# Optimization experiments

Hardware: AMD Instinct MI355X
Metric: run time of the kernel (lower is better)

The kernel has to match this reference:

```python
import jax, jax.numpy as jnp
import numpy as np

N = 50000      # areaNum
E = 64         # embeddingsize
NE = 800000    # nonzeros of normalized adjacency
WK = 9         # walk_length + 1
L = 2          # args.L
TMP = 0.5      # args.choosing_tmp
BIAS = 1e-4


def _logistic_noise(k, shape):
    # eps ~ U(bias, 1-bias); noise = log(eps) - log(1-eps)
    u = jax.random.uniform(k, shape, minval=BIAS, maxval=1.0 - BIAS)
    return jnp.log(u) - jnp.log1p(-u)


def setup_inputs() -> dict:
    key = jax.random.key(0)
    ks = jax.random.split(key, 16)
    rng = np.random.default_rng(0)

    # ---- normalized sparse adjacency (D^-1/2 A D^-1/2), COO sorted by row ----
    row = np.sort(rng.integers(0, N, NE))
    col = rng.integers(0, N, NE)
    deg = np.bincount(row, minlength=N).astype(np.float32)
    dinv = np.where(deg > 0, deg ** -0.5, 0.0).astype(np.float32)
    vals = dinv[row] * dinv[col]

    # ---- random-walk mean-pooling adjacency, row-normalized ----
    rw_row = np.repeat(np.arange(N), WK)
    rw_col = rng.integers(0, N, N * WK)
    rw_col[::WK] = np.arange(N)  # walk starts at self
    rw_vals = np.full(N * WK, 1.0 / WK, dtype=np.float32)

    def lin(k, fan_in, shape):
        return jax.random.normal(k, shape, dtype=jnp.float32) / np.sqrt(fan_in)

    inp = {
        'x': jax.random.normal(ks[0], (N, E), dtype=jnp.float32),
        'vals': jnp.asarray(vals),
        'rw_vals': jnp.asarray(rw_vals),
        't_W1': lin(ks[1], 2 * E, (L, 2 * E, E)),
        't_b1': jnp.zeros((L, E), jnp.float32),
        't_W2': lin(ks[2], E, (L, E, 1)),
        't_b2': jnp.zeros((L, 1), jnp.float32),
        's_W1': lin(ks[3], E, (L, E, E)),
        's_b1': jnp.zeros((L, E), jnp.float32),
        's_W2': lin(ks[4], E, (L, E, 1)),
        's_b2': jnp.zeros((L, 1), jnp.float32),
        't_noise': _logistic_noise(ks[5], (L, NE)),
        's_noise': _logistic_noise(ks[6], (L, N, 1)),
        'row': jnp.asarray(row, dtype=jnp.int64) if jax.config.jax_enable_x64 else jnp.asarray(row, dtype=jnp.int32),
        'col': jnp.asarray(col, dtype=jnp.int32),
        'rw_row': jnp.asarray(rw_row, dtype=jnp.int32),
        'rw_col': jnp.asarray(rw_col, dtype=jnp.int32),
    }
    inp['row'] = jnp.asarray(row, dtype=jnp.int32)
    return inp


def reference(x, vals, rw_vals, t_W1, t_b1, t_W2, t_b2, s_W1, s_b1, s_W2, s_b2,
              t_noise, s_noise, row, col, rw_row, rw_col):
    n = x.shape[0]

    def spmm(r, c, v, h):  # sparse [n,n] @ dense [n,E]
        return jax.ops.segment_sum(v[:, None] * h[c], r, num_segments=n)

    # per-edge concat of ORIGINAL embeddings (same tensor every layer, as in source)
    t_cat = jnp.concatenate([x[row], x[col]], axis=-1)  # [nE, 2E]

    # --- mask-learning pass ---
    cur = x
    t_masks, s_masks = [], []
    for i in range(L):
        cur = spmm(row, col, vals, cur)
        t_h = jax.nn.relu(t_cat @ t_W1[i] + t_b1[i])
        t_logit = t_h @ t_W2[i] + t_b2[i]                      # [nE,1]
        t_m = jax.nn.sigmoid((t_noise[i][:, None] + t_logit) / TMP)[:, 0]
        t_masks.append(t_m)
        s_h = jax.nn.relu(cur @ s_W1[i] + s_b1[i])
        s_logit = s_h @ s_W2[i] + s_b2[i]                      # [N,1]
        s_masks.append(jax.nn.sigmoid((s_noise[i] + s_logit) / TMP))

    # --- t branch: gated spmm propagation, mean over layers ---
    cur_t = x
    acc_t = x
    for i in range(L):
        cur_t = spmm(row, col, vals * t_masks[i], cur_t)
        acc_t = acc_t + cur_t
    emb_t = acc_t / (L + 1)

    # --- s branch: gated mix with random-walk mean pooling, then spmm ---
    cur_s = x
    acc_s = x
    s_reg = jnp.float32(0.0)
    for i in range(L):
        mp = spmm(rw_row, rw_col, rw_vals, cur_s)
        cur_s = s_masks[i] * cur_s + (1.0 - s_masks[i]) * mp
        cur_s = spmm(row, col, vals, cur_s)
        acc_s = acc_s + cur_s
        s_reg = s_reg + s_masks[i].sum() / n
    emb_s = acc_s / (L + 1)
    s_reg = s_reg / L
    t_reg = jnp.float32(0.0)  # source never accumulates into t_reg
    return emb_t, emb_s, t_reg, s_reg, t_masks[-1]
```

## Files before the change

kernel.cpp:

```cpp
#include <hip/hip_runtime.h>

#define NNODES 50000
#define EDIM 64
#define WKLEN 9
#define NEDGE 800000
#define NPAD (NNODES + 64)

using bf16x8 = __attribute__((ext_vector_type(8))) __bf16;
using f32x4  = __attribute__((ext_vector_type(4))) float;

__device__ __align__(256) unsigned short g_xbf[NPAD * EDIM];
__device__ __align__(256) unsigned short g_ABh[NNODES * 128];
__device__ __align__(256) unsigned short g_c1h[NPAD * EDIM];
__device__ __align__(256) unsigned short g_c2h[NPAD * EDIM];
__device__ __align__(256) unsigned short g_g0h[NNODES * EDIM];
__device__ __align__(256) unsigned short g_sc1h[NNODES * EDIM];
__device__ __align__(256) unsigned short g_Pr[NNODES * 128];
__device__ __align__(256) unsigned short g_Pc[NNODES * 128];
__device__ __align__(256) float g_mt0[NEDGE];
__device__ __align__(256) float g_mt1[NEDGE];
__device__ __align__(256) float g_sm0[NNODES];
__device__ __align__(256) float g_sm1[NNODES];
__device__ __align__(256) int   g_rowptr[NNODES + 1];
__device__ __align__(256) unsigned short g_Tswz[2048 * 8];
__device__ __align__(256) unsigned short g_Sswz[1024 * 8];

__device__ __forceinline__ unsigned short f2bf(float f) {
    union { float f; unsigned int i; } v;
    v.f = f;
    unsigned int r = v.i + 0x7FFFu + ((v.i >> 16) & 1u);
    return (unsigned short)(r >> 16);
}
__device__ __forceinline__ float bf2f_lo(unsigned int u) {
    union { unsigned int i; float f; } v; v.i = u << 16; return v.f;
}
__device__ __forceinline__ float bf2f_hi(unsigned int u) {
    union { unsigned int i; float f; } v; v.i = u & 0xFFFF0000u; return v.f;
}

__global__ __launch_bounds__(256) void misc_kernel(
    const float* __restrict__ x, const float* __restrict__ tW1,
    const float* __restrict__ sW1, const int* __restrict__ row,
    int n, int nE)
{
    int bid = blockIdx.x, tid = threadIdx.x;
    if (bid < 1563) {
        int i = bid * 256 + tid;
        if (i < NNODES * EDIM / 8) {
            const float* src = x + i * 8;
            union { unsigned short s[8]; uint4 q; } u;
#pragma unroll
            for (int j = 0; j < 8; ++j) u.s[j] = f2bf(src[j]);
            *(uint4*)&g_xbf[i * 8] = u.q;
        }
    } else if (bid < 1759) {
        int i = (bid - 1563) * 256 + tid;
        if (i > n) return;
        int lo = 0, hi = nE;
        while (lo < hi) {
            int mid = (lo + hi) >> 1;
            if (row[mid] < i) lo = mid + 1; else hi = mid;
        }
        g_rowptr[i] = lo;
    } else if (bid < 1767) {
        int t = (bid - 1759) * 256 + tid;
        int s = t >> 9, f = (t >> 6) & 7, ln = t & 63;
        int li = s >> 1, half = s & 1, ks = f >> 2, nn = f & 3;
        int q = ln >> 4, mcl = ln & 15;
        union { unsigned short sv[8]; uint4 q4; } u;
#pragma unroll
        for (int j = 0; j < 8; ++j) {
            int kg = half * 64 + ks * 32 + q * 8 + j;
            u.sv[j] = f2bf(tW1[li * 8192 + kg * 64 + nn * 16 + mcl]);
        }
        *(uint4*)&g_Tswz[t * 8] = u.q4;
    } else {
        int t = (bid - 1767) * 256 + tid;
        int li = t >> 9, ks = (t >> 8) & 1, nn = (t >> 6) & 3, ln = t & 63;
        int q = ln >> 4, mcl = ln & 15;
        union { unsigned short sv[8]; uint4 q4; } u;
#pragma unroll
        for (int j = 0; j < 8; ++j)
            u.sv[j] = f2bf(sW1[li * 4096 + (ks * 32 + q * 8 + j) * 64 + nn * 16 + mcl]);
        *(uint4*)&g_Sswz[t * 8] = u.q4;
    }
}

__global__ __launch_bounds__(256) void prep2_kernel(int n)
{
    int tid = threadIdx.x;
    int wave = tid >> 6, lane = tid & 63;
    int mc = lane & 15, quad = lane >> 4;
    int nb = blockIdx.x * 64 + wave * 16;
    const unsigned short* bp = g_xbf + (nb + mc) * 64 + quad * 8;
    bf16x8 af0 = *(const bf16x8*)bp;
    bf16x8 af1 = *(const bf16x8*)(bp + 32);
    const f32x4 zero = {0.f, 0.f, 0.f, 0.f};
#pragma unroll
    for (int s = 0; s < 4; ++s) {
        int li = s >> 1, half = s & 1;
        f32x4 acc[4];
#pragma unroll
        for (int nn = 0; nn < 4; ++nn) acc[nn] = zero;
#pragma unroll
        for (int nn = 0; nn < 4; ++nn) {
            bf16x8 b0 = *(const bf16x8*)&g_Tswz[((s * 8 + nn) * 64 + lane) * 8];
            bf16x8 b1 = *(const bf16x8*)&g_Tswz[((s * 8 + 4 + nn) * 64 + lane) * 8];
            acc[nn] = __builtin_amdgcn_mfma_f32_16x16x32_bf16(af0, b0, acc[nn], 0, 0, 0);
            acc[nn] = __builtin_amdgcn_mfma_f32_16x16x32_bf16(af1, b1, acc[nn], 0, 0, 0);
        }
        unsigned short* dst = half ? g_Pc : g_Pr;
#pragma unroll
        for (int nn = 0; nn < 4; ++nn)
#pragma unroll
            for (int r = 0; r < 4; ++r) {
                int node = nb + quad * 4 + r;
                if (node < n)
                    dst[node * 128 + li * 64 + nn * 16 + mc] = f2bf(acc[nn][r]);
            }
    }
}

__global__ __launch_bounds__(256) void edge_mask_kernel(
    const float* __restrict__ tb1, const float* __restrict__ tW2,
    const float* __restrict__ tb2, const float* __restrict__ tnoise,
    const int* __restrict__ row, const int* __restrict__ col,
    float* __restrict__ mask_out, int nE)
{
    int tid = threadIdx.x;
    int lane = tid & 63;
    int sub = lane & 7;
    int eg = lane >> 3;
    int wv = (blockIdx.x * 256 + tid) >> 6;
    int e = wv * 8 + eg;

    float b1_0[8], b1_1[8], w2_0[8], w2_1[8];
    *(float4*)&b1_0[0] = *(const float4*)&tb1[sub * 8];
    *(float4*)&b1_0[4] = *(const float4*)&tb1[sub * 8 + 4];
    *(float4*)&b1_1[0] = *(const float4*)&tb1[64 + sub * 8];
    *(float4*)&b1_1[4] = *(const float4*)&tb1[64 + sub * 8 + 4];
    *(float4*)&w2_0[0] = *(const float4*)&tW2[sub * 8];
    *(float4*)&w2_0[4] = *(const float4*)&tW2[sub * 8 + 4];
    *(float4*)&w2_1[0] = *(const float4*)&tW2[64 + sub * 8];
    *(float4*)&w2_1[4] = *(const float4*)&tW2[64 + sub * 8 + 4];

    int rn = row[e], cn = col[e];
    uint4 qr0 = *(const uint4*)&g_Pr[rn * 128 + sub * 8];
    uint4 qr1 = *(const uint4*)&g_Pr[rn * 128 + 64 + sub * 8];
    uint4 qc0 = *(const uint4*)&g_Pc[cn * 128 + sub * 8];
    uint4 qc1 = *(const uint4*)&g_Pc[cn * 128 + 64 + sub * 8];

    float p0 = 0.f, p1 = 0.f;
    unsigned r0[4] = {qr0.x, qr0.y, qr0.z, qr0.w};
    unsigned r1[4] = {qr1.x, qr1.y, qr1.z, qr1.w};
    unsigned c0[4] = {qc0.x, qc0.y, qc0.z, qc0.w};
    unsigned c1[4] = {qc1.x, qc1.y, qc1.z, qc1.w};
#pragma unroll
    for (int k = 0; k < 4; ++k) {
        float hA = fmaxf(bf2f_lo(r0[k]) + bf2f_lo(c0[k]) + b1_0[2 * k], 0.f);
        float hB = fmaxf(bf2f_hi(r0[k]) + bf2f_hi(c0[k]) + b1_0[2 * k + 1], 0.f);
        p0 = fmaf(hA, w2_0[2 * k], p0);
        p0 = fmaf(hB, w2_0[2 * k + 1], p0);
        float gA = fmaxf(bf2f_lo(r1[k]) + bf2f_lo(c1[k]) + b1_1[2 * k], 0.f);
        float gB = fmaxf(bf2f_hi(r1[k]) + bf2f_hi(c1[k]) + b1_1[2 * k + 1], 0.f);
        p1 = fmaf(gA, w2_1[2 * k], p1);
        p1 = fmaf(gB, w2_1[2 * k + 1], p1);
    }
#pragma unroll
    for (int off = 1; off <= 4; off <<= 1) {
        p0 += __shfl_xor(p0, off, 64);
        p1 += __shfl_xor(p1, off, 64);
    }
    if (sub == 0) {
        float z0 = (tnoise[e] + p0 + tb2[0]) * 2.0f;
        float m0 = 1.0f / (1.0f + expf(-z0));
        g_mt0[e] = m0;
        float z1 = (tnoise[nE + e] + p1 + tb2[1]) * 2.0f;
        float m1 = 1.0f / (1.0f + expf(-z1));
        g_mt1[e] = m1;
        mask_out[e] = m1;
    }
}

__device__ __forceinline__ void nm_body(
    int bid, const unsigned short* __restrict__ cur, int li,
    const float* __restrict__ b1, const float* __restrict__ W2,
    const float* __restrict__ b2, const float* __restrict__ noise,
    float* __restrict__ smout, int n)
{
    int tid = threadIdx.x;
    int wave = tid >> 6, lane = tid & 63;
    int mc = lane & 15, quad = lane >> 4;
    int nb = bid * 64 + wave * 16;
    const unsigned short* basep = cur + (nb + mc) * 64 + quad * 8;
    bf16x8 af0 = *(const bf16x8*)basep;
    bf16x8 af1 = *(const bf16x8*)(basep + 32);
    f32x4 acc[4];
    const f32x4 zero = {0.f, 0.f, 0.f, 0.f};
#pragma unroll
    for (int nn = 0; nn < 4; ++nn) acc[nn] = zero;
#pragma unroll
    for (int nn = 0; nn < 4; ++nn) {
        bf16x8 b0 = *(const bf16x8*)&g_Sswz[((li * 8 + nn) * 64 + lane) * 8];
        bf16x8 b1f = *(const bf16x8*)&g_Sswz[((li * 8 + 4 + nn) * 64 + lane) * 8];
        acc[nn] = __builtin_amdgcn_mfma_f32_16x16x32_bf16(af0, b0, acc[nn], 0, 0, 0);
        acc[nn] = __builtin_amdgcn_mfma_f32_16x16x32_bf16(af1, b1f, acc[nn], 0, 0, 0);
    }
    float p[4];
#pragma unroll
    for (int r = 0; r < 4; ++r) {
        float s = 0.f;
#pragma unroll
        for (int nn = 0; nn < 4; ++nn) {
            float h = acc[nn][r] + b1[nn * 16 + mc];
            s = fmaf(fmaxf(h, 0.f), W2[nn * 16 + mc], s);
        }
        p[r] = s;
    }
#pragma unroll
    for (int off = 8; off >= 1; off >>= 1)
#pragma unroll
        for (int r = 0; r < 4; ++r) p[r] += __shfl_xor(p[r], off, 64);
    if (mc == 0) {
        float b2v = b2[0];
#pragma unroll
        for (int r = 0; r < 4; ++r) {
            int node = nb + quad * 4 + r;
            if (node < n) {
                float z = (noise[node] + p[r] + b2v) * 2.0f;
                smout[node] = 1.0f / (1.0f + expf(-z));
            }
        }
    }
}

__global__ __launch_bounds__(256) void s1_kernel(
    const int* __restrict__ colv, const float* __restrict__ vals, int n)
{
    int w = (blockIdx.x * 256 + threadIdx.x) >> 6;
    int lane = threadIdx.x & 63;
    int el = lane >> 5, d2 = lane & 31;
    int s = g_rowptr[w], e = g_rowptr[w + 1];
    float p0 = 0.f, p1 = 0.f, q0 = 0.f, q1 = 0.f;
    float P0 = 0.f, P1 = 0.f, Q0 = 0.f, Q1 = 0.f;
    int j = s + el;
    for (; j + 2 < e; j += 4) {
        int cA = colv[j];      float vA = vals[j];     float mA = g_mt0[j];
        int cB = colv[j + 2];  float vB = vals[j + 2]; float mB = g_mt0[j + 2];
        unsigned uA = *(const unsigned*)&g_xbf[cA * 64 + 2 * d2];
        unsigned uB = *(const unsigned*)&g_xbf[cB * 64 + 2 * d2];
        float a0 = bf2f_lo(uA), a1 = bf2f_hi(uA);
        float bb0 = bf2f_lo(uB), bb1 = bf2f_hi(uB);
        float vmA = vA * mA, vmB = vB * mB;
        p0 = fmaf(vA, a0, p0);  p1 = fmaf(vA, a1, p1);
        q0 = fmaf(vmA, a0, q0); q1 = fmaf(vmA, a1, q1);
        P0 = fmaf(vB, bb0, P0);  P1 = fmaf(vB, bb1, P1);
        Q0 = fmaf(vmB, bb0, Q0); Q1 = fmaf(vmB, bb1, Q1);
    }
    for (; j < e; j += 2) {
        int c = colv[j]; float v = vals[j], m = g_mt0[j];
        unsigned u = *(const unsigned*)&g_xbf[c * 64 + 2 * d2];
        float a0 = bf2f_lo(u), a1 = bf2f_hi(u);
        float vm = v * m;
        p0 = fmaf(v, a0, p0);  p1 = fmaf(v, a1, p1);
        q0 = fmaf(vm, a0, q0); q1 = fmaf(vm, a1, q1);
    }
    p0 += P0; p1 += P1; q0 += Q0; q1 += Q1;
    p0 += __shfl_xor(p0, 32, 64); p1 += __shfl_xor(p1, 32, 64);
    q0 += __shfl_xor(q0, 32, 64); q1 += __shfl_xor(q1, 32, 64);
    if (el == 0) {
        uint2 pk;
        pk.x = (unsigned)f2bf(p0) | ((unsigned)f2bf(q0) << 16);
        pk.y = (unsigned)f2bf(p1) | ((unsigned)f2bf(q1) << 16);
        *(uint2*)&g_ABh[w * 128 + 4 * d2] = pk;
        *(unsigned*)&g_c1h[w * 64 + 2 * d2] =
            (unsigned)f2bf(p0) | ((unsigned)f2bf(p1) << 16);
    }
}

__global__ __launch_bounds__(256) void s2_nm0_kernel(
    const int* __restrict__ colv, const float* __restrict__ vals,
    const float* __restrict__ x, float* __restrict__ emb_t,
    const float* __restrict__ sb1, const float* __restrict__ sW2,
    const float* __restrict__ sb2, const float* __restrict__ snz, int n)
{
    if (blockIdx.x >= 12500) {
        nm_body(blockIdx.x - 12500, g_c1h, 0, sb1, sW2, sb2, snz, g_sm0, n);
        return;
    }
    int w = (blockIdx.x * 256 + threadIdx.x) >> 6;
    int lane = threadIdx.x & 63;
    int el = lane >> 5, d2 = lane & 31;
    int s = g_rowptr[w], e = g_rowptr[w + 1];
    float c0 = 0.f, c1 = 0.f, t0 = 0.f, t1 = 0.f;
    float C0 = 0.f, C1 = 0.f, T0 = 0.f, T1 = 0.f;
    int j = s + el;
    for (; j + 2 < e; j += 4) {
        int cA = colv[j];      float vA = vals[j];     float mA = g_mt1[j];
        int cB = colv[j + 2];  float vB = vals[j + 2]; float mB = g_mt1[j + 2];
        uint2 UA = *(const uint2*)&g_ABh[cA * 128 + 4 * d2];
        uint2 UB = *(const uint2*)&g_ABh[cB * 128 + 4 * d2];
        float vmA = vA * mA, vmB = vB * mB;
        c0 = fmaf(vA, bf2f_lo(UA.x), c0); t0 = fmaf(vmA, bf2f_hi(UA.x), t0);
        c1 = fmaf(vA, bf2f_lo(UA.y), c1); t1 = fmaf(vmA, bf2f_hi(UA.y), t1);
        C0 = fmaf(vB, bf2f_lo(UB.x), C0); T0 = fmaf(vmB, bf2f_hi(UB.x), T0);
        C1 = fmaf(vB, bf2f_lo(UB.y), C1); T1 = fmaf(vmB, bf2f_hi(UB.y), T1);
    }
    for (; j < e; j += 2) {
        int c = colv[j]; float v = vals[j], m = g_mt1[j];
        uint2 U = *(const uint2*)&g_ABh[c * 128 + 4 * d2];
        float vm = v * m;
        c0 = fmaf(v, bf2f_lo(U.x), c0); t0 = fmaf(vm, bf2f_hi(U.x), t0);
        c1 = fmaf(v, bf2f_lo(U.y), c1); t1 = fmaf(vm, bf2f_hi(U.y), t1);
    }
    c0 += C0; c1 += C1; t0 += T0; t1 += T1;
    c0 += __shfl_xor(c0, 32, 64); c1 += __shfl_xor(c1, 32, 64);
    t0 += __shfl_xor(t0, 32, 64); t1 += __shfl_xor(t1, 32, 64);
    if (el == 0) {
        int o2 = w * 64 + 2 * d2;
        uint2 U2 = *(const uint2*)&g_ABh[w * 128 + 4 * d2];
        float2 et;
        et.x = (x[o2]     + bf2f_hi(U2.x) + t0) * (1.0f / 3.0f);
        et.y = (x[o2 + 1] + bf2f_hi(U2.y) + t1) * (1.0f / 3.0f);
        *(float2*)&emb_t[o2] = et;
        *(unsigned*)&g_c2h[o2] = (unsigned)f2bf(c0) | ((unsigned)f2bf(c1) << 16);
    }
}

__device__ __forceinline__ void rw_body(
    int bid, const int* __restrict__ rw_col, const float* __restrict__ rwv,
    const unsigned short* __restrict__ cur, const float* __restrict__ smask,
    unsigned short* __restrict__ outg)
{
    int w = (bid * 256 + threadIdx.x) >> 6;
    int lane = threadIdx.x & 63;
    int el = lane >> 5, d2 = lane & 31;
    int base = w * WKLEN;
    float a0 = 0.f, a1 = 0.f;
    for (int j = el; j < WKLEN; j += 2) {
        int c = rw_col[base + j];
        float v = rwv[base + j];
        unsigned u = *(const unsigned*)&cur[c * 64 + 2 * d2];
        a0 = fmaf(v, bf2f_lo(u), a0);
        a1 = fmaf(v, bf2f_hi(u), a1);
    }
    a0 += __shfl_xor(a0, 32, 64);
    a1 += __shfl_xor(a1, 32, 64);
    if (el == 0) {
        float sm = smask[w];
        unsigned u = *(const unsigned*)&cur[w * 64 + 2 * d2];
        float r0 = sm * bf2f_lo(u) + (1.f - sm) * a0;
        float r1 = sm * bf2f_hi(u) + (1.f - sm) * a1;
        *(unsigned*)&outg[w * 64 + 2 * d2] =
            (unsigned)f2bf(r0) | ((unsigned)f2bf(r1) << 16);
    }
}

__global__ __launch_bounds__(256) void rw0_nm1_kernel(
    const int* __restrict__ rw_col, const float* __restrict__ rwv,
    const float* __restrict__ sb1, const float* __restrict__ sW2,
    const float* __restrict__ sb2, const float* __restrict__ snz, int n)
{
    if (blockIdx.x >= 12500) {
        nm_body(blockIdx.x - 12500, g_c2h, 1, sb1, sW2, sb2, snz, g_sm1, n);
        return;
    }
    rw_body(blockIdx.x, rw_col, rwv, g_xbf, g_sm0, g_g0h);
}

__global__ __launch_bounds__(256) void spmm10_kernel(
    const int* __restrict__ colv, const float* __restrict__ vals, int n)
{
    int w = (blockIdx.x * 256 + threadIdx.x) >> 6;
    int lane = threadIdx.x & 63;
    int el = lane >> 5, d2 = lane & 31;
    int s = g_rowptr[w], e = g_rowptr[w + 1];
    float a0 = 0.f, a1 = 0.f, A0 = 0.f, A1 = 0.f;
    int j = s + el;
    for (; j + 2 < e; j += 4) {
        int cA = colv[j];     float vA = vals[j];
        int cB = colv[j + 2]; float vB = vals[j + 2];
        unsigned uA = *(const unsigned*)&g_g0h[cA * 64 + 2 * d2];
        unsigned uB = *(const unsigned*)&g_g0h[cB * 64 + 2 * d2];
        a0 = fmaf(vA, bf2f_lo(uA), a0); a1 = fmaf(vA, bf2f_hi(uA), a1);
        A0 = fmaf(vB, bf2f_lo(uB), A0); A1 = fmaf(vB, bf2f_hi(uB), A1);
    }
    for (; j < e; j += 2) {
        int c = colv[j]; float v = vals[j];
        unsigned u = *(const unsigned*)&g_g0h[c * 64 + 2 * d2];
        a0 = fmaf(v, bf2f_lo(u), a0); a1 = fmaf(v, bf2f_hi(u), a1);
    }
    a0 += A0; a1 += A1;
    a0 += __shfl_xor(a0, 32, 64); a1 += __shfl_xor(a1, 32, 64);
    if (el == 0)
        *(unsigned*)&g_sc1h[w * 64 + 2 * d2] =
            (unsigned)f2bf(a0) | ((unsigned)f2bf(a1) << 16);
}

__global__ __launch_bounds__(256) void rw1_kernel(
    const int* __restrict__ rw_col, const float* __restrict__ rwv)
{
    rw_body(blockIdx.x, rw_col, rwv, g_sc1h, g_sm1, g_g0h);
}

__global__ __launch_bounds__(256) void spmm12_fin_kernel(
    const int* __restrict__ colv, const float* __restrict__ vals,
    const float* __restrict__ x, float* __restrict__ emb_s,
    float* __restrict__ out, int n)
{
    if (blockIdx.x >= 12500) {
        __shared__ float red[256];
        float s = 0.f;
        for (int i = threadIdx.x; i < n; i += 256) s += g_sm0[i] + g_sm1[i];
        red[threadIdx.x] = s;
        __syncthreads();
        for (int off = 128; off >= 1; off >>= 1) {
            if (threadIdx.x < off) red[threadIdx.x] += red[threadIdx.x + off];
            __syncthreads();
        }
        if (threadIdx.x == 0) {
            out[6400000] = 0.0f;
            out[6400001] = red[0] / (2.0f * n);
        }
        return;
    }
    int w = (blockIdx.x * 256 + threadIdx.x) >> 6;
    int lane = threadIdx.x & 63;
    int el = lane >> 5, d2 = lane & 31;
    int s = g_rowptr[w], e = g_rowptr[w + 1];
    float a0 = 0.f, a1 = 0.f, A0 = 0.f, A1 = 0.f;
    int j = s + el;
    for (; j + 2 < e; j += 4) {
        int cA = colv[j];     float vA = vals[j];
        int cB = colv[j + 2]; float vB = vals[j + 2];
        unsigned uA = *(const unsigned*)&g_g0h[cA * 64 + 2 * d2];
        unsigned uB = *(const unsigned*)&g_g0h[cB * 64 + 2 * d2];
        a0 = fmaf(vA, bf2f_lo(uA), a0); a1 = fmaf(vA, bf2f_hi(uA), a1);
        A0 = fmaf(vB, bf2f_lo(uB), A0); A1 = fmaf(vB, bf2f_hi(uB), A1);
    }
    for (; j < e; j += 2) {
        int c = colv[j]; float v = vals[j];
        unsigned u = *(const unsigned*)&g_g0h[c * 64 + 2 * d2];
        a0 = fmaf(v, bf2f_lo(u), a0); a1 = fmaf(v, bf2f_hi(u), a1);
    }
    a0 += A0; a1 += A1;
    a0 += __shfl_xor(a0, 32, 64); a1 += __shfl_xor(a1, 32, 64);
    if (el == 0) {
        int o2 = w * 64 + 2 * d2;
        unsigned uc = *(const unsigned*)&g_sc1h[o2];
        float2 es;
        es.x = (x[o2]     + bf2f_lo(uc) + a0) * (1.0f / 3.0f);
        es.y = (x[o2 + 1] + bf2f_hi(uc) + a1) * (1.0f / 3.0f);
        *(float2*)&emb_s[o2] = es;
    }
}

extern "C" void kernel_launch(void* const* d_in, const int* in_sizes, int n_in,
                              void* d_out, int out_size, void* d_ws, size_t ws_size,
                              hipStream_t stream)
{
    const float* x    = (const float*)d_in[0];
    const float* vals = (const float*)d_in[1];
    const float* rwv  = (const float*)d_in[2];
    const float* tW1  = (const float*)d_in[3];
    const float* tb1  = (const float*)d_in[4];
    const float* tW2  = (const float*)d_in[5];
    const float* tb2  = (const float*)d_in[6];
    const float* sW1  = (const float*)d_in[7];
    const float* sb1  = (const float*)d_in[8];
    const float* sW2  = (const float*)d_in[9];
    const float* sb2  = (const float*)d_in[10];
    const float* tnz  = (const float*)d_in[11];
    const float* snz  = (const float*)d_in[12];
    const int* row   = (const int*)d_in[13];
    const int* colv  = (const int*)d_in[14];
    const int* rwcol = (const int*)d_in[16];

    const int n = NNODES;
    const int nE = in_sizes[1];

    float* out   = (float*)d_out;
    float* emb_t = out;
    float* emb_s = out + 3200000;
    float* masko = out + 6400002;

    misc_kernel<<<1771, 256, 0, stream>>>(x, tW1, sW1, row, n, nE);
    prep2_kernel<<<782, 256, 0, stream>>>(n);
    edge_mask_kernel<<<nE / 32, 256, 0, stream>>>(tb1, tW2, tb2, tnz,
                                                  row, colv, masko, nE);
    s1_kernel<<<12500, 256, 0, stream>>>(colv, vals, n);
    s2_nm0_kernel<<<12500 + 782, 256, 0, stream>>>(colv, vals, x, emb_t,
                                                   sb1, sW2, sb2, snz, n);
    rw0_nm1_kernel<<<12500 + 782, 256, 0, stream>>>(rwcol, rwv,
                                                    sb1 + 64, sW2 + 64, sb2 + 1,
                                                    snz + n, n);
    spmm10_kernel<<<12500, 256, 0, stream>>>(colv, vals, n);
    rw1_kernel<<<12500, 256, 0, stream>>>(rwcol, rwv);
    spmm12_fin_kernel<<<12501, 256, 0, stream>>>(colv, vals, x, emb_s, out, n);
}
```

Measured before the change: 408.6 us.

## Map one half-wave per row in SpMM kernels, drop cross-half shuffle

Every gather-based SpMM and random-walk kernel now assigns 32 lanes (half a wavefront) to each node row instead of a full 64-lane wavefront that split edges between the two halves. Each half-wave walks all edges of its row with a 4-way unrolled loop and four independent accumulator sets, so the final shuffle reduction and the el==0 guard on stores go away. Grid sizes are halved to match, and a shared spmm_body helper is factored out. The change is meant to cut wasted lanes and reduction overhead at an average of about 16 edges per row, at the cost of longer serial loops per row and more register pressure.

```diff
diff --git a/kernel.cpp b/kernel.cpp
--- a/kernel.cpp
+++ b/kernel.cpp
@@ -237,45 +237,47 @@
 __global__ __launch_bounds__(256) void s1_kernel(
     const int* __restrict__ colv, const float* __restrict__ vals, int n)
 {
-    int w = (blockIdx.x * 256 + threadIdx.x) >> 6;
-    int lane = threadIdx.x & 63;
-    int el = lane >> 5, d2 = lane & 31;
+    int w = blockIdx.x * 8 + (threadIdx.x >> 5);
+    int d2 = threadIdx.x & 31;
     int s = g_rowptr[w], e = g_rowptr[w + 1];
-    float p0 = 0.f, p1 = 0.f, q0 = 0.f, q1 = 0.f;
-    float P0 = 0.f, P1 = 0.f, Q0 = 0.f, Q1 = 0.f;
-    int j = s + el;
-    for (; j + 2 < e; j += 4) {
-        int cA = colv[j];      float vA = vals[j];     float mA = g_mt0[j];
-        int cB = colv[j + 2];  float vB = vals[j + 2]; float mB = g_mt0[j + 2];
-        unsigned uA = *(const unsigned*)&g_xbf[cA * 64 + 2 * d2];
-        unsigned uB = *(const unsigned*)&g_xbf[cB * 64 + 2 * d2];
-        float a0 = bf2f_lo(uA), a1 = bf2f_hi(uA);
-        float bb0 = bf2f_lo(uB), bb1 = bf2f_hi(uB);
-        float vmA = vA * mA, vmB = vB * mB;
-        p0 = fmaf(vA, a0, p0);  p1 = fmaf(vA, a1, p1);
-        q0 = fmaf(vmA, a0, q0); q1 = fmaf(vmA, a1, q1);
-        P0 = fmaf(vB, bb0, P0);  P1 = fmaf(vB, bb1, P1);
-        Q0 = fmaf(vmB, bb0, Q0); Q1 = fmaf(vmB, bb1, Q1);
-    }
-    for (; j < e; j += 2) {
+    float pl[4] = {0.f, 0.f, 0.f, 0.f}, ph[4] = {0.f, 0.f, 0.f, 0.f};
+    float ql[4] = {0.f, 0.f, 0.f, 0.f}, qh[4] = {0.f, 0.f, 0.f, 0.f};
+    int j = s;
+    for (; j + 3 < e; j += 4) {
+        int c0 = colv[j], c1 = colv[j + 1], c2 = colv[j + 2], c3 = colv[j + 3];
+        unsigned u0 = *(const unsigned*)&g_xbf[c0 * 64 + 2 * d2];
+        unsigned u1 = *(const unsigned*)&g_xbf[c1 * 64 + 2 * d2];
+        unsigned u2 = *(const unsigned*)&g_xbf[c2 * 64 + 2 * d2];
+        unsigned u3 = *(const unsigned*)&g_xbf[c3 * 64 + 2 * d2];
+        float v0 = vals[j], v1 = vals[j + 1], v2 = vals[j + 2], v3 = vals[j + 3];
+        float m0 = g_mt0[j], m1 = g_mt0[j + 1], m2 = g_mt0[j + 2], m3 = g_mt0[j + 3];
+        float vm0 = v0 * m0, vm1 = v1 * m1, vm2 = v2 * m2, vm3 = v3 * m3;
+        pl[0] = fmaf(v0, bf2f_lo(u0), pl[0]); ph[0] = fmaf(v0, bf2f_hi(u0), ph[0]);
+        ql[0] = fmaf(vm0, bf2f_lo(u0), ql[0]); qh[0] = fmaf(vm0, bf2f_hi(u0), qh[0]);
+        pl[1] = fmaf(v1, bf2f_lo(u1), pl[1]); ph[1] = fmaf(v1, bf2f_hi(u1), ph[1]);
+        ql[1] = fmaf(vm1, bf2f_lo(u1), ql[1]); qh[1] = fmaf(vm1, bf2f_hi(u1), qh[1]);
+        pl[2] = fmaf(v2, bf2f_lo(u2), pl[2]); ph[2] = fmaf(v2, bf2f_hi(u2), ph[2]);
+        ql[2] = fmaf(vm2, bf2f_lo(u2), ql[2]); qh[2] = fmaf(vm2, bf2f_hi(u2), qh[2]);
+        pl[3] = fmaf(v3, bf2f_lo(u3), pl[3]); ph[3] = fmaf(v3, bf2f_hi(u3), ph[3]);
+        ql[3] = fmaf(vm3, bf2f_lo(u3), ql[3]); qh[3] = fmaf(vm3, bf2f_hi(u3), qh[3]);
+    }
+    for (; j < e; ++j) {
         int c = colv[j]; float v = vals[j], m = g_mt0[j];
         unsigned u = *(const unsigned*)&g_xbf[c * 64 + 2 * d2];
-        float a0 = bf2f_lo(u), a1 = bf2f_hi(u);
         float vm = v * m;
-        p0 = fmaf(v, a0, p0);  p1 = fmaf(v, a1, p1);
-        q0 = fmaf(vm, a0, q0); q1 = fmaf(vm, a1, q1);
-    }
-    p0 += P0; p1 += P1; q0 += Q0; q1 += Q1;
-    p0 += __shfl_xor(p0, 32, 64); p1 += __shfl_xor(p1, 32, 64);
-    q0 += __shfl_xor(q0, 32, 64); q1 += __shfl_xor(q1, 32, 64);
-    if (el == 0) {
-        uint2 pk;
-        pk.x = (unsigned)f2bf(p0) | ((unsigned)f2bf(q0) << 16);
-        pk.y = (unsigned)f2bf(p1) | ((unsigned)f2bf(q1) << 16);
-        *(uint2*)&g_ABh[w * 128 + 4 * d2] = pk;
-        *(unsigned*)&g_c1h[w * 64 + 2 * d2] =
-            (unsigned)f2bf(p0) | ((unsigned)f2bf(p1) << 16);
-    }
+        pl[0] = fmaf(v, bf2f_lo(u), pl[0]); ph[0] = fmaf(v, bf2f_hi(u), ph[0]);
+        ql[0] = fmaf(vm, bf2f_lo(u), ql[0]); qh[0] = fmaf(vm, bf2f_hi(u), qh[0]);
+    }
+    float p0 = (pl[0] + pl[1]) + (pl[2] + pl[3]);
+    float p1 = (ph[0] + ph[1]) + (ph[2] + ph[3]);
+    float q0 = (ql[0] + ql[1]) + (ql[2] + ql[3]);
+    float q1 = (qh[0] + qh[1]) + (qh[2] + qh[3]);
+    uint2 pk;
+    pk.x = (unsigned)f2bf(p0) | ((unsigned)f2bf(q0) << 16);
+    pk.y = (unsigned)f2bf(p1) | ((unsigned)f2bf(q1) << 16);
+    *(uint2*)&g_ABh[w * 128 + 4 * d2] = pk;
+    *(unsigned*)&g_c1h[w * 64 + 2 * d2] =
+        (unsigned)f2bf(p0) | ((unsigned)f2bf(p1) << 16);
 }
 
 __global__ __launch_bounds__(256) void s2_nm0_kernel(
@@ -284,47 +286,52 @@
     const float* __restrict__ sb1, const float* __restrict__ sW2,
     const float* __restrict__ sb2, const float* __restrict__ snz, int n)
 {
-    if (blockIdx.x >= 12500) {
-        nm_body(blockIdx.x - 12500, g_c1h, 0, sb1, sW2, sb2, snz, g_sm0, n);
+    if (blockIdx.x >= 6250) {
+        nm_body(blockIdx.x - 6250, g_c1h, 0, sb1, sW2, sb2, snz, g_sm0, n);
         return;
     }
-    int w = (blockIdx.x * 256 + threadIdx.x) >> 6;
-    int lane = threadIdx.x & 63;
-    int el = lane >> 5, d2 = lane & 31;
+    int w = blockIdx.x * 8 + (threadIdx.x >> 5);
+    int d2 = threadIdx.x & 31;
     int s = g_rowptr[w], e = g_rowptr[w + 1];
-    float c0 = 0.f, c1 = 0.f, t0 = 0.f, t1 = 0.f;
-    float C0 = 0.f, C1 = 0.f, T0 = 0.f, T1 = 0.f;
-    int j = s + el;
-    for (; j + 2 < e; j += 4) {
-        int cA = colv[j];      float vA = vals[j];     float mA = g_mt1[j];
-        int cB = colv[j + 2];  float vB = vals[j + 2]; float mB = g_mt1[j + 2];
-        uint2 UA = *(const uint2*)&g_ABh[cA * 128 + 4 * d2];
-        uint2 UB = *(const uint2*)&g_ABh[cB * 128 + 4 * d2];
-        float vmA = vA * mA, vmB = vB * mB;
-        c0 = fmaf(vA, bf2f_lo(UA.x), c0); t0 = fmaf(vmA, bf2f_hi(UA.x), t0);
-        c1 = fmaf(vA, bf2f_lo(UA.y), c1); t1 = fmaf(vmA, bf2f_hi(UA.y), t1);
-        C0 = fmaf(vB, bf2f_lo(UB.x), C0); T0 = fmaf(vmB, bf2f_hi(UB.x), T0);
-        C1 = fmaf(vB, bf2f_lo(UB.y), C1); T1 = fmaf(vmB, bf2f_hi(UB.y), T1);
-    }
-    for (; j < e; j += 2) {
+    float cl[4] = {0.f, 0.f, 0.f, 0.f}, ch[4] = {0.f, 0.f, 0.f, 0.f};
+    float tl[4] = {0.f, 0.f, 0.f, 0.f}, th[4] = {0.f, 0.f, 0.f, 0.f};
+    int j = s;
+    for (; j + 3 < e; j += 4) {
+        int c0 = colv[j], c1 = colv[j + 1], c2 = colv[j + 2], c3 = colv[j + 3];
+        uint2 U0 = *(const uint2*)&g_ABh[c0 * 128 + 4 * d2];
+        uint2 U1 = *(const uint2*)&g_ABh[c1 * 128 + 4 * d2];
+        uint2 U2 = *(const uint2*)&g_ABh[c2 * 128 + 4 * d2];
+        uint2 U3 = *(const uint2*)&g_ABh[c3 * 128 + 4 * d2];
+        float v0 = vals[j], v1 = vals[j + 1], v2 = vals[j + 2], v3 = vals[j + 3];
+        float m0 = g_mt1[j], m1 = g_mt1[j + 1], m2 = g_mt1[j + 2], m3 = g_mt1[j + 3];
+        float vm0 = v0 * m0, vm1 = v1 * m1, vm2 = v2 * m2, vm3 = v3 * m3;
+        cl[0] = fmaf(v0, bf2f_lo(U0.x), cl[0]); tl[0] = fmaf(vm0, bf2f_hi(U0.x), tl[0]);
+        ch[0] = fmaf(v0, bf2f_lo(U0.y), ch[0]); th[0] = fmaf(vm0, bf2f_hi(U0.y), th[0]);
+        cl[1] = fmaf(v1, bf2f_lo(U1.x), cl[1]); tl[1] = fmaf(vm1, bf2f_hi(U1.x), tl[1]);
+        ch[1] = fmaf(v1, bf2f_lo(U1.y), ch[1]); th[1] = fmaf(vm1, bf2f_hi(U1.y), th[1]);
+        cl[2] = fmaf(v2, bf2f_lo(U2.x), cl[2]); tl[2] = fmaf(vm2, bf2f_hi(U2.x), tl[2]);
+        ch[2] = fmaf(v2, bf2f_lo(U2.y), ch[2]); th[2] = fmaf(vm2, bf2f_hi(U2.y), th[2]);
+        cl[3] = fmaf(v3, bf2f_lo(U3.x), cl[3]); tl[3] = fmaf(vm3, bf2f_hi(U3.x), tl[3]);
+        ch[3] = fmaf(v3, bf2f_lo(U3.y), ch[3]); th[3] = fmaf(vm3, bf2f_hi(U3.y), th[3]);
+    }
+    for (; j < e; ++j) {
         int c = colv[j]; float v = vals[j], m = g_mt1[j];
         uint2 U = *(const uint2*)&g_ABh[c * 128 + 4 * d2];
         float vm = v * m;
-        c0 = fmaf(v, bf2f_lo(U.x), c0); t0 = fmaf(vm, bf2f_hi(U.x), t0);
-        c1 = fmaf(v, bf2f_lo(U.y), c1); t1 = fmaf(vm, bf2f_hi(U.y), t1);
-    }
-    c0 += C0; c1 += C1; t0 += T0; t1 += T1;
-    c0 += __shfl_xor(c0, 32, 64); c1 += __shfl_xor(c1, 32, 64);
-    t0 += __shfl_xor(t0, 32, 64); t1 += __shfl_xor(t1, 32, 64);
-    if (el == 0) {
-        int o2 = w * 64 + 2 * d2;
-        uint2 U2 = *(const uint2*)&g_ABh[w * 128 + 4 * d2];
-        float2 et;
-        et.x = (x[o2]     + bf2f_hi(U2.x) + t0) * (1.0f / 3.0f);
-        et.y = (x[o2 + 1] + bf2f_hi(U2.y) + t1) * (1.0f / 3.0f);
-        *(float2*)&emb_t[o2] = et;
-        *(unsigned*)&g_c2h[o2] = (unsigned)f2bf(c0) | ((unsigned)f2bf(c1) << 16);
-    }
+        cl[0] = fmaf(v, bf2f_lo(U.x), cl[0]); tl[0] = fmaf(vm, bf2f_hi(U.x), tl[0]);
+        ch[0] = fmaf(v, bf2f_lo(U.y), ch[0]); th[0] = fmaf(vm, bf2f_hi(U.y), th[0]);
+    }
+    float c0s = (cl[0] + cl[1]) + (cl[2] + cl[3]);
+    float c1s = (ch[0] + ch[1]) + (ch[2] + ch[3]);
+    float t0s = (tl[0] + tl[1]) + (tl[2] + tl[3]);
+    float t1s = (th[0] + th[1]) + (th[2] + th[3]);
+    int o2 = w * 64 + 2 * d2;
+    uint2 U2v = *(const uint2*)&g_ABh[w * 128 + 4 * d2];
+    float2 et;
+    et.x = (x[o2]     + bf2f_hi(U2v.x) + t0s) * (1.0f / 3.0f);
+    et.y = (x[o2 + 1] + bf2f_hi(U2v.y) + t1s) * (1.0f / 3.0f);
+    *(float2*)&emb_t[o2] = et;
+    *(unsigned*)&g_c2h[o2] = (unsigned)f2bf(c0s) | ((unsigned)f2bf(c1s) << 16);
 }
 
 __device__ __forceinline__ void rw_body(
@@ -332,28 +339,24 @@
     const unsigned short* __restrict__ cur, const float* __restrict__ smask,
     unsigned short* __restrict__ outg)
 {
-    int w = (bid * 256 + threadIdx.x) >> 6;
-    int lane = threadIdx.x & 63;
-    int el = lane >> 5, d2 = lane & 31;
+    int w = bid * 8 + (threadIdx.x >> 5);
+    int d2 = threadIdx.x & 31;
     int base = w * WKLEN;
     float a0 = 0.f, a1 = 0.f;
-    for (int j = el; j < WKLEN; j += 2) {
+#pragma unroll
+    for (int j = 0; j < WKLEN; ++j) {
         int c = rw_col[base + j];
         float v = rwv[base + j];
         unsigned u = *(const unsigned*)&cur[c * 64 + 2 * d2];
         a0 = fmaf(v, bf2f_lo(u), a0);
         a1 = fmaf(v, bf2f_hi(u), a1);
     }
-    a0 += __shfl_xor(a0, 32, 64);
-    a1 += __shfl_xor(a1, 32, 64);
-    if (el == 0) {
-        float sm = smask[w];
-        unsigned u = *(const unsigned*)&cur[w * 64 + 2 * d2];
-        float r0 = sm * bf2f_lo(u) + (1.f - sm) * a0;
-        float r1 = sm * bf2f_hi(u) + (1.f - sm) * a1;
-        *(unsigned*)&outg[w * 64 + 2 * d2] =
-            (unsigned)f2bf(r0) | ((unsigned)f2bf(r1) << 16);
-    }
+    float sm = smask[w];
+    unsigned u = *(const unsigned*)&cur[w * 64 + 2 * d2];
+    float r0 = sm * bf2f_lo(u) + (1.f - sm) * a0;
+    float r1 = sm * bf2f_hi(u) + (1.f - sm) * a1;
+    *(unsigned*)&outg[w * 64 + 2 * d2] =
+        (unsigned)f2bf(r0) | ((unsigned)f2bf(r1) << 16);
 }
 
 __global__ __launch_bounds__(256) void rw0_nm1_kernel(
@@ -361,40 +364,52 @@
     const float* __restrict__ sb1, const float* __restrict__ sW2,
     const float* __restrict__ sb2, const float* __restrict__ snz, int n)
 {
-    if (blockIdx.x >= 12500) {
-        nm_body(blockIdx.x - 12500, g_c2h, 1, sb1, sW2, sb2, snz, g_sm1, n);
+    if (blockIdx.x >= 6250) {
+        nm_body(blockIdx.x - 6250, g_c2h, 1, sb1, sW2, sb2, snz, g_sm1, n);
         return;
     }
     rw_body(blockIdx.x, rw_col, rwv, g_xbf, g_sm0, g_g0h);
+}
+
+__device__ __forceinline__ void spmm_body(
+    int bid, const int* __restrict__ colv, const float* __restrict__ vals,
+    const unsigned short* __restrict__ h, float* __restrict__ l0,
+    float* __restrict__ l1, int* __restrict__ wout, int* __restrict__ d2out)
+{
+    int w = bid * 8 + (threadIdx.x >> 5);
+    int d2 = threadIdx.x & 31;
+    int s = g_rowptr[w], e = g_rowptr[w + 1];
+    float al[4] = {0.f, 0.f, 0.f, 0.f}, ah[4] = {0.f, 0.f, 0.f, 0.f};
+    int j = s;
+    for (; j + 3 < e; j += 4) {
+        int c0 = colv[j], c1 = colv[j + 1], c2 = colv[j + 2], c3 = colv[j + 3];
+        unsigned u0 = *(const unsigned*)&h[c0 * 64 + 2 * d2];
+        unsigned u1 = *(const unsigned*)&h[c1 * 64 + 2 * d2];
+        unsigned u2 = *(const unsigned*)&h[c2 * 64 + 2 * d2];
+        unsigned u3 = *(const unsigned*)&h[c3 * 64 + 2 * d2];
+        float v0 = vals[j], v1 = vals[j + 1], v2 = vals[j + 2], v3 = vals[j + 3];
+        al[0] = fmaf(v0, bf2f_lo(u0), al[0]); ah[0] = fmaf(v0, bf2f_hi(u0), ah[0]);
+        al[1] = fmaf(v1, bf2f_lo(u1), al[1]); ah[1] = fmaf(v1, bf2f_hi(u1), ah[1]);
+        al[2] = fmaf(v2, bf2f_lo(u2), al[2]); ah[2] = fmaf(v2, bf2f_hi(u2), ah[2]);
+        al[3] = fmaf(v3, bf2f_lo(u3), al[3]); ah[3] = fmaf(v3, bf2f_hi(u3), ah[3]);
+    }
+    for (; j < e; ++j) {
+        int c = colv[j]; float v = vals[j];
+        unsigned u = *(const unsigned*)&h[c * 64 + 2 * d2];
+        al[0] = fmaf(v, bf2f_lo(u), al[0]); ah[0] = fmaf(v, bf2f_hi(u), ah[0]);
+    }
+    *l0 = (al[0] + al[1]) + (al[2] + al[3]);
+    *l1 = (ah[0] + ah[1]) + (ah[2] + ah[3]);
+    *wout = w; *d2out = d2;
 }
 
 __global__ __launch_bounds__(256) void spmm10_kernel(
     const int* __restrict__ colv, const float* __restrict__ vals, int n)
 {
-    int w = (blockIdx.x * 256 + threadIdx.x) >> 6;
-    int lane = threadIdx.x & 63;
-    int el = lane >> 5, d2 = lane & 31;
-    int s = g_rowptr[w], e = g_rowptr[w + 1];
-    float a0 = 0.f, a1 = 0.f, A0 = 0.f, A1 = 0.f;
-    int j = s + el;
-    for (; j + 2 < e; j += 4) {
-        int cA = colv[j];     float vA = vals[j];
-        int cB = colv[j + 2]; float vB = vals[j + 2];
-        unsigned uA = *(const unsigned*)&g_g0h[cA * 64 + 2 * d2];
-        unsigned uB = *(const unsigned*)&g_g0h[cB * 64 + 2 * d2];
-        a0 = fmaf(vA, bf2f_lo(uA), a0); a1 = fmaf(vA, bf2f_hi(uA), a1);
-        A0 = fmaf(vB, bf2f_lo(uB), A0); A1 = fmaf(vB, bf2f_hi(uB), A1);
-    }
-    for (; j < e; j += 2) {
-        int c = colv[j]; float v = vals[j];
-        unsigned u = *(const unsigned*)&g_g0h[c * 64 + 2 * d2];
-        a0 = fmaf(v, bf2f_lo(u), a0); a1 = fmaf(v, bf2f_hi(u), a1);
-    }
-    a0 += A0; a1 += A1;
-    a0 += __shfl_xor(a0, 32, 64); a1 += __shfl_xor(a1, 32, 64);
-    if (el == 0)
-        *(unsigned*)&g_sc1h[w * 64 + 2 * d2] =
-            (unsigned)f2bf(a0) | ((unsigned)f2bf(a1) << 16);
+    float a0, a1; int w, d2;
+    spmm_body(blockIdx.x, colv, vals, g_g0h, &a0, &a1, &w, &d2);
+    *(unsigned*)&g_sc1h[w * 64 + 2 * d2] =
+        (unsigned)f2bf(a0) | ((unsigned)f2bf(a1) << 16);
 }
 
 __global__ __launch_bounds__(256) void rw1_kernel(
@@ -408,7 +423,7 @@
     const float* __restrict__ x, float* __restrict__ emb_s,
     float* __restrict__ out, int n)
 {
-    if (blockIdx.x >= 12500) {
+    if (blockIdx.x >= 6250) {
         __shared__ float red[256];
         float s = 0.f;
         for (int i = threadIdx.x; i < n; i += 256) s += g_sm0[i] + g_sm1[i];
@@ -424,35 +439,14 @@
         }
         return;
     }
-    int w = (blockIdx.x * 256 + threadIdx.x) >> 6;
-    int lane = threadIdx.x & 63;
-    int el = lane >> 5, d2 = lane & 31;
-    int s = g_rowptr[w], e = g_rowptr[w + 1];
-    float a0 = 0.f, a1 = 0.f, A0 = 0.f, A1 = 0.f;
-    int j = s + el;
-    for (; j + 2 < e; j += 4) {
-        int cA = colv[j];     float vA = vals[j];
-        int cB = colv[j + 2]; float vB = vals[j + 2];
-        unsigned uA = *(const unsigned*)&g_g0h[cA * 64 + 2 * d2];
-        unsigned uB = *(const unsigned*)&g_g0h[cB * 64 + 2 * d2];
-        a0 = fmaf(vA, bf2f_lo(uA), a0); a1 = fmaf(vA, bf2f_hi(uA), a1);
-        A0 = fmaf(vB, bf2f_lo(uB), A0); A1 = fmaf(vB, bf2f_hi(uB), A1);
-    }
-    for (; j < e; j += 2) {
-        int c = colv[j]; float v = vals[j];
-        unsigned u = *(const unsigned*)&g_g0h[c * 64 + 2 * d2];
-        a0 = fmaf(v, bf2f_lo(u), a0); a1 = fmaf(v, bf2f_hi(u), a1);
-    }
-    a0 += A0; a1 += A1;
-    a0 += __shfl_xor(a0, 32, 64); a1 += __shfl_xor(a1, 32, 64);
-    if (el == 0) {
-        int o2 = w * 64 + 2 * d2;
-        unsigned uc = *(const unsigned*)&g_sc1h[o2];
-        float2 es;
-        es.x = (x[o2]     + bf2f_lo(uc) + a0) * (1.0f / 3.0f);
-        es.y = (x[o2 + 1] + bf2f_hi(uc) + a1) * (1.0f / 3.0f);
-        *(float2*)&emb_s[o2] = es;
-    }
+    float a0, a1; int w, d2;
+    spmm_body(blockIdx.x, colv, vals, g_g0h, &a0, &a1, &w, &d2);
+    int o2 = w * 64 + 2 * d2;
+    unsigned uc = *(const unsigned*)&g_sc1h[o2];
+    float2 es;
+    es.x = (x[o2]     + bf2f_lo(uc) + a0) * (1.0f / 3.0f);
+    es.y = (x[o2 + 1] + bf2f_hi(uc) + a1) * (1.0f / 3.0f);
+    *(float2*)&emb_s[o2] = es;
 }
 
 extern "C" void kernel_launch(void* const* d_in, const int* in_sizes, int n_in,
@@ -488,13 +482,13 @@
     prep2_kernel<<<782, 256, 0, stream>>>(n);
     edge_mask_kernel<<<nE / 32, 256, 0, stream>>>(tb1, tW2, tb2, tnz,
                                                   row, colv, masko, nE);
-    s1_kernel<<<12500, 256, 0, stream>>>(colv, vals, n);
-    s2_nm0_kernel<<<12500 + 782, 256, 0, stream>>>(colv, vals, x, emb_t,
-                                                   sb1, sW2, sb2, snz, n);
-    rw0_nm1_kernel<<<12500 + 782, 256, 0, stream>>>(rwcol, rwv,
-                                                    sb1 + 64, sW2 + 64, sb2 + 1,
-                                                    snz + n, n);
-    spmm10_kernel<<<12500, 256, 0, stream>>>(colv, vals, n);
-    rw1_kernel<<<12500, 256, 0, stream>>>(rwcol, rwv);
-    spmm12_fin_kernel<<<12501, 256, 0, stream>>>(colv, vals, x, emb_s, out, n);
-}
+    s1_kernel<<<6250, 256, 0, stream>>>(colv, vals, n);
+    s2_nm0_kernel<<<6250 + 782, 256, 0, stream>>>(colv, vals, x, emb_t,
+                                                  sb1, sW2, sb2, snz, n);
+    rw0_nm1_kernel<<<6250 + 782, 256, 0, stream>>>(rwcol, rwv,
+                                                   sb1 + 64, sW2 + 64, sb2 + 1,
+                                                   snz + n, n);
+    spmm10_kernel<<<6250, 256, 0, stream>>>(colv, vals, n);
+    rw1_kernel<<<6250, 256, 0, stream>>>(rwcol, rwv);
+    spmm12_fin_kernel<<<6251, 256, 0, stream>>>(colv, vals, x, emb_s, out, n);
+}
```

Measured after the change: 352.9 us. -13.6%, faster.
